# Optimization experiments

Hardware: AMD Instinct MI355X
Metric: run time of the kernel (lower is better)

## Reference

```python
import jax, jax.numpy as jnp
import numpy as np
from jax import lax

THETA = 0.7
DN = ('NCHW', 'OIHW', 'NCHW')


def setup_inputs() -> dict:
    key = jax.random.key(0)
    k1, k2 = jax.random.split(key)
    x = jax.random.normal(k1, (16, 64, 128, 128), dtype=jnp.float32)
    W = jax.random.normal(k2, (64, 64, 3, 3), dtype=jnp.float32) * 0.05
    return {"x": x, "W": W}


def _shift_sum(x):
    # Sum of the center view plus the 8 shifted views of the reflection-padded
    # input (the original code's lt/mt/rt/lm/center/mr/ld/md/rd slices cover
    # exactly the full 3x3 neighborhood of the padded tensor).
    B, C, H, W_ = x.shape
    xp = jnp.pad(x, ((0, 0), (0, 0), (1, 1), (1, 1)), mode='reflect')
    s = jnp.zeros_like(x)
    for dy in range(3):
        for dx in range(3):
            s = s + xp[:, :, dy:dy + H, dx:dx + W_]
    return s


def reference(x, W):
    # Conv is linear and bias=False, so sum_i conv(shift_i(x)) == conv(sum_i shift_i(x)).
    s = _shift_sum(x)  # [B,C,H,W]
    out_normal = lax.conv_general_dilated(s, W, (1, 1), [(1, 1), (1, 1)], dimension_numbers=DN)
    kernel_diff = W.sum(axis=(2, 3))[:, :, None, None]  # [C_out,C_in,1,1]
    out_diff = lax.conv_general_dilated(s, kernel_diff, (1, 1), [(0, 0), (0, 0)], dimension_numbers=DN)
    return out_normal - THETA * out_diff
```

## Files before the change

### kernel.cpp

```cpp
#include <hip/hip_runtime.h>
#include <stdint.h>


#define THETA 0.7f

typedef __attribute__((ext_vector_type(8))) short bf16x8;
typedef __attribute__((ext_vector_type(16))) float f32x16;

__device__ inline unsigned short f2bf(float f) {
    unsigned u = __float_as_uint(f);
    u = (u + 0x7FFFu + ((u >> 16) & 1u)) >> 16;
    return (unsigned short)u;
}

__global__ void weff_kernel(const float* __restrict__ W, unsigned short* __restrict__ Wt2) {
    int t = blockIdx.x * blockDim.x + threadIdx.x;
    if (t >= 512) return;
    int o = t >> 3;
    int ch8 = t & 7;
    int c0 = ch8 * 8;
    int ic = ch8 >> 1;
    int mf = o >> 5;
    int lane = (o & 31) | ((ch8 & 1) << 5);

    float v[8][9];
    float tsum[8];
#pragma unroll
    for (int j = 0; j < 8; j++) {
        const float* w = W + ((size_t)o * 64 + c0 + j) * 9;
        float sum = 0.f;
#pragma unroll
        for (int k = 0; k < 9; k++) { v[j][k] = w[k]; sum += v[j][k]; }
        tsum[j] = sum;
    }
#pragma unroll
    for (int tap = 0; tap < 9; tap++) {
        unsigned short* dst = Wt2 + (((size_t)(tap * 4 + ic) * 2 + mf) * 64 + lane) * 8;
#pragma unroll
        for (int j = 0; j < 8; j++) {
            float val = v[j][tap] - ((tap == 4) ? THETA * tsum[j] : 0.f);
            dst[j] = f2bf(val);
        }
    }
}

__global__ __launch_bounds__(512, 4) void fused_kernel(const float* __restrict__ x,
                                                       const unsigned short* __restrict__ Wt2,
                                                       float* __restrict__ out) {
    __shared__ __align__(16) unsigned short sS[4 * 132 * 64];

    int bid = blockIdx.x;
    int b = bid >> 6;
    int h0 = (bid & 63) * 2;
    int tid = threadIdx.x;
    int lane = tid & 63;
    int wv = tid >> 6;
    int n32 = lane & 31;
    int q2 = lane >> 5;
    int ohalf = wv >> 2;
    int orow = (wv >> 1) & 1;
    int whalf = wv & 1;

    int4 z = make_int4(0, 0, 0, 0);
    if (tid < 64) {
        int rr = tid >> 4;
        int sl = ((tid >> 3) & 1) ? 129 : 0;
        int g = tid & 7;
        *(int4*)((char*)sS + ((size_t)(rr * 132 + sl) * 8 + g) * 16) = z;
    }
    if (h0 == 0)
        for (int i = tid; i < 1056; i += 512) *(int4*)((char*)sS + (size_t)i * 16) = z;
    if (h0 == 126)
        for (int i = tid; i < 1056; i += 512) *(int4*)((char*)sS + (size_t)(3168 + i) * 16) = z;

    bf16x8 Af[4], An[4];
#pragma unroll
    for (int ic = 0; ic < 4; ic++)
        Af[ic] = *(const bf16x8*)(Wt2 + (((size_t)(0 * 4 + ic) * 2 + ohalf) * 64 + lane) * 8);

    {
        int w4 = tid & 31;
        int cg = tid >> 5;
        int c0 = cg * 4;
        int u8 = cg >> 1;
        int hh = (cg & 1) * 4;
        const float* xp = x + ((size_t)(b * 64 + c0)) * 16384 + w4 * 4;

        int hgf = (h0 == 0) ? 0 : h0 - 1;
        int hm = (hgf == 0) ? 1 : hgf - 1;
        float4 A[4], Bv[4], C[4];
#pragma unroll
        for (int cc = 0; cc < 4; cc++) {
            A[cc]  = *(const float4*)(xp + (size_t)cc * 16384 + (size_t)hm * 128);
            Bv[cc] = *(const float4*)(xp + (size_t)cc * 16384 + (size_t)hgf * 128);
            C[cc]  = *(const float4*)(xp + (size_t)cc * 16384 + (size_t)(hgf + 1) * 128);
        }

#pragma unroll
        for (int rr = 0; rr < 4; rr++) {
            int hg = h0 - 1 + rr;
            if (hg < 0 || hg > 127) continue;

            float4 Cn[4];
            if (rr < 3) {
                int hn = hg + 2;
                if (hn > 127) hn = 126;
#pragma unroll
                for (int cc = 0; cc < 4; cc++)
                    Cn[cc] = *(const float4*)(xp + (size_t)cc * 16384 + (size_t)hn * 128);
            }

            unsigned short res[4][4];
#pragma unroll
            for (int cc = 0; cc < 4; cc++) {
                float4 vs;
                vs.x = A[cc].x + Bv[cc].x + C[cc].x;
                vs.y = A[cc].y + Bv[cc].y + C[cc].y;
                vs.z = A[cc].z + Bv[cc].z + C[cc].z;
                vs.w = A[cc].w + Bv[cc].w + C[cc].w;
                float L = __shfl_up(vs.w, 1, 32);
                float R = __shfl_down(vs.x, 1, 32);
                float sx = (w4 == 0) ? vs.x + 2.f * vs.y : L + vs.x + vs.y;
                float sy = vs.x + vs.y + vs.z;
                float sz = vs.y + vs.z + vs.w;
                float sw_ = (w4 == 31) ? 2.f * vs.z + vs.w : vs.z + vs.w + R;
                res[cc][0] = f2bf(sx);
                res[cc][1] = f2bf(sy);
                res[cc][2] = f2bf(sz);
                res[cc][3] = f2bf(sw_);
            }
#pragma unroll
            for (int k = 0; k < 4; k++) {
                int slot = w4 * 4 + k + 1;
                ushort4 o4 = make_ushort4(res[0][k], res[1][k], res[2][k], res[3][k]);
                *(ushort4*)(sS + (size_t)(rr * 132 + slot) * 64 + ((u8 ^ (slot & 7)) << 3) + hh) = o4;
            }
            if (rr < 3) {
#pragma unroll
                for (int cc = 0; cc < 4; cc++) { A[cc] = Bv[cc]; Bv[cc] = C[cc]; C[cc] = Cn[cc]; }
            }
        }
    }
    __syncthreads();

    int p0[3][4];
#pragma unroll
    for (int kx = 0; kx < 3; kx++)
#pragma unroll
        for (int ic = 0; ic < 4; ic++) {
            int slot = n32 + kx + whalf * 64;
            int g = (ic * 2 + q2) ^ (slot & 7);
            p0[kx][ic] = slot * 64 + g * 8;
        }

    f32x16 acc[2];
#pragma unroll
    for (int nf = 0; nf < 2; nf++)
#pragma unroll
        for (int r = 0; r < 16; r++) acc[nf][r] = 0.f;

#pragma unroll
    for (int tap = 0; tap < 9; tap++) {
        int ky = tap / 3, kx = tap % 3;
        if (tap < 8) {
#pragma unroll
            for (int ic = 0; ic < 4; ic++)
                An[ic] = *(const bf16x8*)(Wt2 + (((size_t)((tap + 1) * 4 + ic) * 2 + ohalf) * 64 + lane) * 8);
        }
#pragma unroll
        for (int ic = 0; ic < 4; ic++) {
            const unsigned short* bp = sS + (size_t)(orow + ky) * 8448 + p0[kx][ic];
            bf16x8 b0 = *(const bf16x8*)(bp);
            bf16x8 b1 = *(const bf16x8*)(bp + 2048);
            acc[0] = __builtin_amdgcn_mfma_f32_32x32x16_bf16(Af[ic], b0, acc[0], 0, 0, 0);
            acc[1] = __builtin_amdgcn_mfma_f32_32x32x16_bf16(Af[ic], b1, acc[1], 0, 0, 0);
        }
        if (tap < 8) {
#pragma unroll
            for (int k = 0; k < 4; k++) Af[k] = An[k];
        }
    }

    float* ob = out + ((size_t)b * 64) * 16384 + (size_t)(h0 + orow) * 128 + whalf * 64;
#pragma unroll
    for (int nf = 0; nf < 2; nf++)
#pragma unroll
        for (int r = 0; r < 16; r++) {
            int o = ohalf * 32 + (r & 3) + 8 * (r >> 2) + 4 * q2;
            ob[(size_t)o * 16384 + nf * 32 + n32] = acc[nf][r];
        }
}

extern "C" void kernel_launch(void* const* d_in, const int* in_sizes, int n_in,
                              void* d_out, int out_size, void* d_ws, size_t ws_size,
                              hipStream_t stream) {
    const float* x = (const float*)d_in[0];
    const float* W = (const float*)d_in[1];
    float* outp = (float*)d_out;

    unsigned short* Wt2 = (unsigned short*)d_ws;

    weff_kernel<<<2, 256, 0, stream>>>(W, Wt2);
    fused_kernel<<<1024, 512, 0, stream>>>(x, Wt2, outp);
}
```

Before: 141.2 us.

## Prefetch LDS operands, add second swizzle term, packed bf16 convert, remap blocks

Result: faster. 136.4 us (-3.4%).

```diff
diff --git a/kernel.cpp b/kernel.cpp
--- a/kernel.cpp
+++ b/kernel.cpp
@@ -11,6 +11,11 @@
     unsigned u = __float_as_uint(f);
     u = (u + 0x7FFFu + ((u >> 16) & 1u)) >> 16;
     return (unsigned short)u;
+}
+__device__ inline unsigned cvt_pk_bf16(float lo, float hi) {
+    unsigned r;
+    asm volatile("v_cvt_pk_bf16_f32 %0, %1, %2" : "=v"(r) : "v"(lo), "v"(hi));
+    return r;
 }
 
 __global__ void weff_kernel(const float* __restrict__ W, unsigned short* __restrict__ Wt2) {
@@ -49,7 +54,8 @@
                                                        float* __restrict__ out) {
     __shared__ __align__(16) unsigned short sS[4 * 132 * 64];
 
-    int bid = blockIdx.x;
+    int bid0 = blockIdx.x;
+    int bid = (bid0 & 7) * 128 + (bid0 >> 3);
     int b = bid >> 6;
     int h0 = (bid & 63) * 2;
     int tid = threadIdx.x;
@@ -73,11 +79,6 @@
     if (h0 == 126)
         for (int i = tid; i < 1056; i += 512) *(int4*)((char*)sS + (size_t)(3168 + i) * 16) = z;
 
-    bf16x8 Af[4], An[4];
-#pragma unroll
-    for (int ic = 0; ic < 4; ic++)
-        Af[ic] = *(const bf16x8*)(Wt2 + (((size_t)(0 * 4 + ic) * 2 + ohalf) * 64 + lane) * 8);
-
     {
         int w4 = tid & 31;
         int cg = tid >> 5;
@@ -110,7 +111,7 @@
                     Cn[cc] = *(const float4*)(xp + (size_t)cc * 16384 + (size_t)hn * 128);
             }
 
-            unsigned short res[4][4];
+            float rf[4][4];
 #pragma unroll
             for (int cc = 0; cc < 4; cc++) {
                 float4 vs;
@@ -120,20 +121,18 @@
                 vs.w = A[cc].w + Bv[cc].w + C[cc].w;
                 float L = __shfl_up(vs.w, 1, 32);
                 float R = __shfl_down(vs.x, 1, 32);
-                float sx = (w4 == 0) ? vs.x + 2.f * vs.y : L + vs.x + vs.y;
-                float sy = vs.x + vs.y + vs.z;
-                float sz = vs.y + vs.z + vs.w;
-                float sw_ = (w4 == 31) ? 2.f * vs.z + vs.w : vs.z + vs.w + R;
-                res[cc][0] = f2bf(sx);
-                res[cc][1] = f2bf(sy);
-                res[cc][2] = f2bf(sz);
-                res[cc][3] = f2bf(sw_);
+                rf[cc][0] = (w4 == 0) ? vs.x + 2.f * vs.y : L + vs.x + vs.y;
+                rf[cc][1] = vs.x + vs.y + vs.z;
+                rf[cc][2] = vs.y + vs.z + vs.w;
+                rf[cc][3] = (w4 == 31) ? 2.f * vs.z + vs.w : vs.z + vs.w + R;
             }
 #pragma unroll
             for (int k = 0; k < 4; k++) {
                 int slot = w4 * 4 + k + 1;
-                ushort4 o4 = make_ushort4(res[0][k], res[1][k], res[2][k], res[3][k]);
-                *(ushort4*)(sS + (size_t)(rr * 132 + slot) * 64 + ((u8 ^ (slot & 7)) << 3) + hh) = o4;
+                uint2 o2 = make_uint2(cvt_pk_bf16(rf[0][k], rf[1][k]),
+                                      cvt_pk_bf16(rf[2][k], rf[3][k]));
+                int p = u8 ^ (slot & 7) ^ ((slot >> 2) & 7);
+                *(uint2*)(sS + (size_t)(rr * 132 + slot) * 64 + (p << 3) + hh) = o2;
             }
             if (rr < 3) {
 #pragma unroll
@@ -149,7 +148,7 @@
 #pragma unroll
         for (int ic = 0; ic < 4; ic++) {
             int slot = n32 + kx + whalf * 64;
-            int g = (ic * 2 + q2) ^ (slot & 7);
+            int g = (ic * 2 + q2) ^ (slot & 7) ^ ((slot >> 2) & 7);
             p0[kx][ic] = slot * 64 + g * 8;
         }
 
@@ -158,26 +157,39 @@
     for (int nf = 0; nf < 2; nf++)
 #pragma unroll
         for (int r = 0; r < 16; r++) acc[nf][r] = 0.f;
+
+    bf16x8 Af[4], An[4], B0[4], B0n[4], B1[4];
+#pragma unroll
+    for (int ic = 0; ic < 4; ic++) {
+        Af[ic] = *(const bf16x8*)(Wt2 + (((size_t)(0 * 4 + ic) * 2 + ohalf) * 64 + lane) * 8);
+        B0[ic] = *(const bf16x8*)(sS + (size_t)(orow + 0) * 8448 + p0[0][ic]);
+    }
 
 #pragma unroll
     for (int tap = 0; tap < 9; tap++) {
         int ky = tap / 3, kx = tap % 3;
+        const unsigned short* brow = sS + (size_t)(orow + ky) * 8448;
+#pragma unroll
+        for (int ic = 0; ic < 4; ic++)
+            B1[ic] = *(const bf16x8*)(brow + p0[kx][ic] + 2048);
         if (tap < 8) {
-#pragma unroll
-            for (int ic = 0; ic < 4; ic++)
+            int kyn = (tap + 1) / 3, kxn = (tap + 1) % 3;
+            const unsigned short* brn = sS + (size_t)(orow + kyn) * 8448;
+#pragma unroll
+            for (int ic = 0; ic < 4; ic++) {
+                B0n[ic] = *(const bf16x8*)(brn + p0[kxn][ic]);
                 An[ic] = *(const bf16x8*)(Wt2 + (((size_t)((tap + 1) * 4 + ic) * 2 + ohalf) * 64 + lane) * 8);
-        }
-#pragma unroll
-        for (int ic = 0; ic < 4; ic++) {
-            const unsigned short* bp = sS + (size_t)(orow + ky) * 8448 + p0[kx][ic];
-            bf16x8 b0 = *(const bf16x8*)(bp);
-            bf16x8 b1 = *(const bf16x8*)(bp + 2048);
-            acc[0] = __builtin_amdgcn_mfma_f32_32x32x16_bf16(Af[ic], b0, acc[0], 0, 0, 0);
-            acc[1] = __builtin_amdgcn_mfma_f32_32x32x16_bf16(Af[ic], b1, acc[1], 0, 0, 0);
-        }
+            }
+        }
+#pragma unroll
+        for (int ic = 0; ic < 4; ic++)
+            acc[0] = __builtin_amdgcn_mfma_f32_32x32x16_bf16(Af[ic], B0[ic], acc[0], 0, 0, 0);
+#pragma unroll
+        for (int ic = 0; ic < 4; ic++)
+            acc[1] = __builtin_amdgcn_mfma_f32_32x32x16_bf16(Af[ic], B1[ic], acc[1], 0, 0, 0);
         if (tap < 8) {
 #pragma unroll
-            for (int k = 0; k < 4; k++) Af[k] = An[k];
+            for (int k = 0; k < 4; k++) { Af[k] = An[k]; B0[k] = B0n[k]; }
         }
     }
 
```
